# Optimization experiments

Hardware: AMD Instinct MI355X
Metric: run time of the kernel (lower is better)

Reference implementation:

```python
import jax, jax.numpy as jnp
import numpy as np

N_ENT = 15000  # entity id range; also used for relation ids in this synthetic setup

def _triple_key(h, r, t):
    # Unique int64 key per (h, r, t) triple; max ~15000^3 < 2^63.
    return (h * N_ENT + r) * N_ENT + t

def setup_inputs() -> dict:
    key = jax.random.key(0)
    k1, k2, k3, k4 = jax.random.split(key, 4)
    Q, N = 100000, 10000000
    heads = jax.random.randint(k1, (Q,), 0, N_ENT, dtype=jnp.int64)
    rels = jax.random.randint(k2, (Q,), 0, N_ENT, dtype=jnp.int64)
    tails = jax.random.randint(k3, (Q,), 0, N_ENT, dtype=jnp.int64)
    data = jax.random.randint(k4, (3, N), 0, N_ENT, dtype=jnp.int64)
    return {"heads": heads, "rels": rels, "tails": tails, "data": data}

def reference(heads, rels, tails, data) -> jnp.ndarray:
    # Faithful to PerfeCT.forward: response[i] = 1 iff (heads[i], rels[i], tails[i])
    # appears as a row of data.T; output = 10 * (response - 0.5).
    data_keys = jnp.sort(_triple_key(data[0], data[1], data[2]))  # [N]
    q_keys = _triple_key(heads, rels, tails)                       # [Q]
    idx = jnp.searchsorted(data_keys, q_keys)
    idx = jnp.clip(idx, 0, data_keys.shape[0] - 1)
    member = (data_keys[idx] == q_keys).astype(jnp.float32)        # [Q]
    return 10.0 * (member - 0.5)
```

## Files before the change

kernel.cpp:

```cpp
#include <hip/hip_runtime.h>
#include <stdint.h>


#define EMPTY64     0xFFFFFFFFFFFFFFFFULL
#define BLOOM_WORDS 16384u
#define BLOOM_MASK  (BLOOM_WORDS - 1u)

__device__ __forceinline__ uint32_t key32(uint32_t h, uint32_t r, uint32_t t) {
    return (h * 15000u + r) * 15000u + t;
}

__device__ __forceinline__ uint64_t mix64(uint64_t x) {
    x ^= x >> 30; x *= 0xbf58476d1ce4e5b9ULL;
    x ^= x >> 27; x *= 0x94d049bb133111ebULL;
    x ^= x >> 31;
    return x;
}

__global__ void clear_ws(uint4* __restrict__ table4, unsigned n_table4,
                         uint4* __restrict__ bloom4, unsigned n_bloom4) {
    unsigned i = blockIdx.x * blockDim.x + threadIdx.x;
    if (i < n_table4) table4[i] = make_uint4(~0u, ~0u, ~0u, ~0u);
    if (i < n_bloom4) bloom4[i] = make_uint4(0u, 0u, 0u, 0u);
}

__global__ void insert_queries(const int* __restrict__ heads,
                               const int* __restrict__ rels,
                               const int* __restrict__ tails,
                               unsigned long long* __restrict__ table,
                               unsigned tmask,
                               uint32_t* __restrict__ g_bloom,
                               float* __restrict__ out,
                               int Q) {
    int i = blockIdx.x * blockDim.x + threadIdx.x;
    if (i >= Q) return;
    out[i] = -5.0f;
    uint32_t key = key32((uint32_t)heads[i], (uint32_t)rels[i], (uint32_t)tails[i]);
    uint64_t mix = mix64(key);
    uint32_t bm = (1u << ((mix >> 46) & 31u)) | (1u << ((mix >> 51) & 31u));
    atomicOr(&g_bloom[(mix >> 32) & BLOOM_MASK], bm);
    uint64_t entry = (uint64_t)key | ((uint64_t)(unsigned)i << 32);
    unsigned slot = (unsigned)mix & tmask;
    for (unsigned step = 0; step <= tmask; ++step) {
        if (atomicCAS(&table[slot], EMPTY64, (unsigned long long)entry) == EMPTY64) break;
        slot = (slot + 1u) & tmask;
    }
}

__device__ __forceinline__ void probe_one(uint32_t key,
                                          const unsigned long long* __restrict__ table,
                                          unsigned tmask,
                                          const uint32_t* lbloom,
                                          float* __restrict__ out) {
    uint64_t mix = mix64(key);
    uint32_t w  = lbloom[(mix >> 32) & BLOOM_MASK];
    uint32_t bm = (1u << ((mix >> 46) & 31u)) | (1u << ((mix >> 51) & 31u));
    if ((w & bm) != bm) return;
    unsigned slot = (unsigned)mix & tmask;
    for (unsigned step = 0; step <= tmask; ++step) {
        unsigned long long e = table[slot];
        if (e == EMPTY64) break;
        if ((uint32_t)e == key) out[e >> 32] = 5.0f;
        slot = (slot + 1u) & tmask;
    }
}

__global__ __launch_bounds__(1024) void scan_data(const int* __restrict__ data, int N,
                                                  const unsigned long long* __restrict__ table,
                                                  unsigned tmask,
                                                  const uint32_t* __restrict__ g_bloom,
                                                  float* __restrict__ out) {
    __shared__ uint32_t bloom[BLOOM_WORDS];
    {
        const uint4* src = (const uint4*)g_bloom;
        uint4* dst = (uint4*)bloom;
        for (unsigned w = threadIdx.x; w < BLOOM_WORDS / 4; w += blockDim.x)
            dst[w] = src[w];
    }
    __syncthreads();

    const unsigned tid    = blockIdx.x * blockDim.x + threadIdx.x;
    const unsigned stride = gridDim.x * blockDim.x;

    if ((N & 3) == 0) {
        const int nq = N >> 2;
        const uint4* h4 = (const uint4*)data;
        const uint4* r4 = (const uint4*)(data + (size_t)N);
        const uint4* t4 = (const uint4*)(data + 2 * (size_t)N);
        for (unsigned q = tid; q < (unsigned)nq; q += stride) {
            uint4 h = h4[q], r = r4[q], t = t4[q];
            probe_one(key32(h.x, r.x, t.x), table, tmask, bloom, out);
            probe_one(key32(h.y, r.y, t.y), table, tmask, bloom, out);
            probe_one(key32(h.z, r.z, t.z), table, tmask, bloom, out);
            probe_one(key32(h.w, r.w, t.w), table, tmask, bloom, out);
        }
    } else {
        for (unsigned i = tid; i < (unsigned)N; i += stride) {
            probe_one(key32((uint32_t)data[i],
                            (uint32_t)data[(size_t)N + i],
                            (uint32_t)data[2 * (size_t)N + i]),
                      table, tmask, bloom, out);
        }
    }
}

extern "C" void kernel_launch(void* const* d_in, const int* in_sizes, int n_in,
                              void* d_out, int out_size, void* d_ws, size_t ws_size,
                              hipStream_t stream) {
    const int* heads = (const int*)d_in[0];
    const int* rels  = (const int*)d_in[1];
    const int* tails = (const int*)d_in[2];
    const int* data  = (const int*)d_in[3];
    float* out = (float*)d_out;

    const int Q = in_sizes[0];
    const int N = in_sizes[3] / 3;

    size_t cap = 1ull << 18;
    if (cap * 8 + BLOOM_WORDS * 4 > ws_size) cap = 1ull << 17;
    if (cap * 8 + BLOOM_WORDS * 4 > ws_size) return;
    unsigned tmask = (unsigned)(cap - 1);
    unsigned long long* table = (unsigned long long*)d_ws;
    uint32_t* g_bloom = (uint32_t*)((char*)d_ws + cap * 8);

    {
        unsigned n_table4 = (unsigned)(cap / 2);
        unsigned n_bloom4 = BLOOM_WORDS / 4;
        unsigned n = n_table4 > n_bloom4 ? n_table4 : n_bloom4;
        dim3 block(256), grid((n + 255) / 256);
        clear_ws<<<grid, block, 0, stream>>>((uint4*)table, n_table4,
                                             (uint4*)g_bloom, n_bloom4);
    }
    {
        dim3 block(256), grid((Q + 255) / 256);
        insert_queries<<<grid, block, 0, stream>>>(heads, rels, tails, table, tmask,
                                                   g_bloom, out, Q);
    }
    {
        dim3 block(1024), grid(512);
        scan_data<<<grid, block, 0, stream>>>(data, N, table, tmask, g_bloom, out);
    }
}
```

Baseline: 225.5 us.

## Probe hash table in 16-byte pairs with interleaved bloom checks and nontemporal loads

Insertion now starts at even slots, so probes can read two adjacent 8-byte entries as one 16-byte load and stop early when either entry is empty. The four keys per thread are hashed and bloom-tested together, then probed in one interleaved loop, which raises memory-level parallelism. Streaming data loads use nontemporal hints so they do not pollute the cache, and launch bounds are tightened. In exchange the probe chains are walked pairwise, and there is more control divergence per thread.

```diff
diff --git a/kernel.cpp b/kernel.cpp
--- a/kernel.cpp
+++ b/kernel.cpp
@@ -5,6 +5,9 @@
 #define EMPTY64     0xFFFFFFFFFFFFFFFFULL
 #define BLOOM_WORDS 16384u
 #define BLOOM_MASK  (BLOOM_WORDS - 1u)
+
+typedef unsigned int       v4u   __attribute__((ext_vector_type(4)));
+typedef unsigned long long v2u64 __attribute__((ext_vector_type(2)));
 
 __device__ __forceinline__ uint32_t key32(uint32_t h, uint32_t r, uint32_t t) {
     return (h * 15000u + r) * 15000u + t;
@@ -40,36 +43,33 @@
     uint32_t bm = (1u << ((mix >> 46) & 31u)) | (1u << ((mix >> 51) & 31u));
     atomicOr(&g_bloom[(mix >> 32) & BLOOM_MASK], bm);
     uint64_t entry = (uint64_t)key | ((uint64_t)(unsigned)i << 32);
-    unsigned slot = (unsigned)mix & tmask;
+    unsigned slot = ((unsigned)mix & (tmask >> 1)) << 1;
     for (unsigned step = 0; step <= tmask; ++step) {
         if (atomicCAS(&table[slot], EMPTY64, (unsigned long long)entry) == EMPTY64) break;
         slot = (slot + 1u) & tmask;
     }
 }
 
-__device__ __forceinline__ void probe_one(uint32_t key,
-                                          const unsigned long long* __restrict__ table,
-                                          unsigned tmask,
-                                          const uint32_t* lbloom,
-                                          float* __restrict__ out) {
-    uint64_t mix = mix64(key);
-    uint32_t w  = lbloom[(mix >> 32) & BLOOM_MASK];
-    uint32_t bm = (1u << ((mix >> 46) & 31u)) | (1u << ((mix >> 51) & 31u));
-    if ((w & bm) != bm) return;
-    unsigned slot = (unsigned)mix & tmask;
-    for (unsigned step = 0; step <= tmask; ++step) {
-        unsigned long long e = table[slot];
-        if (e == EMPTY64) break;
-        if ((uint32_t)e == key) out[e >> 32] = 5.0f;
-        slot = (slot + 1u) & tmask;
+__device__ __forceinline__ void probe_pairs(uint32_t key, unsigned b,
+                                            const v2u64* __restrict__ tb,
+                                            unsigned bmask,
+                                            float* __restrict__ out) {
+    for (unsigned step = 0; step <= bmask; ++step) {
+        v2u64 e = tb[b];
+        bool le = (e.x == EMPTY64), he = (e.y == EMPTY64);
+        if (!le && (uint32_t)e.x == key) out[e.x >> 32] = 5.0f;
+        if (!he && (uint32_t)e.y == key) out[e.y >> 32] = 5.0f;
+        if (le || he) return;
+        b = (b + 1u) & bmask;
     }
 }
 
-__global__ __launch_bounds__(1024) void scan_data(const int* __restrict__ data, int N,
-                                                  const unsigned long long* __restrict__ table,
-                                                  unsigned tmask,
-                                                  const uint32_t* __restrict__ g_bloom,
-                                                  float* __restrict__ out) {
+__global__ __launch_bounds__(1024, 8)
+void scan_data(const int* __restrict__ data, int N,
+               const unsigned long long* __restrict__ table,
+               unsigned tmask,
+               const uint32_t* __restrict__ g_bloom,
+               float* __restrict__ out) {
     __shared__ uint32_t bloom[BLOOM_WORDS];
     {
         const uint4* src = (const uint4*)g_bloom;
@@ -81,25 +81,74 @@
 
     const unsigned tid    = blockIdx.x * blockDim.x + threadIdx.x;
     const unsigned stride = gridDim.x * blockDim.x;
+    const unsigned bmask  = tmask >> 1;
+    const v2u64* tb = (const v2u64*)table;
 
     if ((N & 3) == 0) {
         const int nq = N >> 2;
-        const uint4* h4 = (const uint4*)data;
-        const uint4* r4 = (const uint4*)(data + (size_t)N);
-        const uint4* t4 = (const uint4*)(data + 2 * (size_t)N);
+        const v4u* h4 = (const v4u*)data;
+        const v4u* r4 = (const v4u*)(data + (size_t)N);
+        const v4u* t4 = (const v4u*)(data + 2 * (size_t)N);
         for (unsigned q = tid; q < (unsigned)nq; q += stride) {
-            uint4 h = h4[q], r = r4[q], t = t4[q];
-            probe_one(key32(h.x, r.x, t.x), table, tmask, bloom, out);
-            probe_one(key32(h.y, r.y, t.y), table, tmask, bloom, out);
-            probe_one(key32(h.z, r.z, t.z), table, tmask, bloom, out);
-            probe_one(key32(h.w, r.w, t.w), table, tmask, bloom, out);
+            v4u h = __builtin_nontemporal_load(&h4[q]);
+            v4u r = __builtin_nontemporal_load(&r4[q]);
+            v4u t = __builtin_nontemporal_load(&t4[q]);
+
+            uint32_t k0 = key32(h.x, r.x, t.x);
+            uint32_t k1 = key32(h.y, r.y, t.y);
+            uint32_t k2 = key32(h.z, r.z, t.z);
+            uint32_t k3 = key32(h.w, r.w, t.w);
+            uint64_t m0 = mix64(k0), m1 = mix64(k1), m2 = mix64(k2), m3 = mix64(k3);
+
+            uint32_t w0 = bloom[(uint32_t)(m0 >> 32) & BLOOM_MASK];
+            uint32_t w1 = bloom[(uint32_t)(m1 >> 32) & BLOOM_MASK];
+            uint32_t w2 = bloom[(uint32_t)(m2 >> 32) & BLOOM_MASK];
+            uint32_t w3 = bloom[(uint32_t)(m3 >> 32) & BLOOM_MASK];
+            uint32_t bm0 = (1u << ((m0 >> 46) & 31u)) | (1u << ((m0 >> 51) & 31u));
+            uint32_t bm1 = (1u << ((m1 >> 46) & 31u)) | (1u << ((m1 >> 51) & 31u));
+            uint32_t bm2 = (1u << ((m2 >> 46) & 31u)) | (1u << ((m2 >> 51) & 31u));
+            uint32_t bm3 = (1u << ((m3 >> 46) & 31u)) | (1u << ((m3 >> 51) & 31u));
+
+            bool d0 = (w0 & bm0) != bm0;
+            bool d1 = (w1 & bm1) != bm1;
+            bool d2 = (w2 & bm2) != bm2;
+            bool d3 = (w3 & bm3) != bm3;
+            unsigned b0 = (unsigned)m0 & bmask;
+            unsigned b1 = (unsigned)m1 & bmask;
+            unsigned b2 = (unsigned)m2 & bmask;
+            unsigned b3 = (unsigned)m3 & bmask;
+
+            for (unsigned g = 0; (g <= bmask) && !(d0 && d1 && d2 && d3); ++g) {
+                v2u64 e0, e1, e2, e3;
+                if (!d0) e0 = tb[b0];
+                if (!d1) e1 = tb[b1];
+                if (!d2) e2 = tb[b2];
+                if (!d3) e3 = tb[b3];
+#define EVAL_PAIR(e, k, b, d)                                              \
+                if (!(d)) {                                                \
+                    bool le = ((e).x == EMPTY64), he = ((e).y == EMPTY64); \
+                    if (!le && (uint32_t)(e).x == (k)) out[(e).x >> 32] = 5.0f; \
+                    if (!he && (uint32_t)(e).y == (k)) out[(e).y >> 32] = 5.0f; \
+                    if (le || he) (d) = true;                              \
+                    else (b) = ((b) + 1u) & bmask;                         \
+                }
+                EVAL_PAIR(e0, k0, b0, d0)
+                EVAL_PAIR(e1, k1, b1, d1)
+                EVAL_PAIR(e2, k2, b2, d2)
+                EVAL_PAIR(e3, k3, b3, d3)
+#undef EVAL_PAIR
+            }
         }
     } else {
         for (unsigned i = tid; i < (unsigned)N; i += stride) {
-            probe_one(key32((uint32_t)data[i],
-                            (uint32_t)data[(size_t)N + i],
-                            (uint32_t)data[2 * (size_t)N + i]),
-                      table, tmask, bloom, out);
+            uint32_t key = key32((uint32_t)data[i],
+                                 (uint32_t)data[(size_t)N + i],
+                                 (uint32_t)data[2 * (size_t)N + i]);
+            uint64_t mix = mix64(key);
+            uint32_t w  = bloom[(uint32_t)(mix >> 32) & BLOOM_MASK];
+            uint32_t bm = (1u << ((mix >> 46) & 31u)) | (1u << ((mix >> 51) & 31u));
+            if ((w & bm) != bm) continue;
+            probe_pairs(key, (unsigned)mix & bmask, tb, bmask, out);
         }
     }
 }
```

New measurement: 212.1 us. -5.9%, faster.
